# Performance work log

Hardware: AMD Instinct MI355X
Metric: run time of the kernel (lower is better)

## Reference

```python
import jax, jax.numpy as jnp
import numpy as np

IN_FEATURES = 4096
OUT_FEATURES = 16384
BATCH, SEQ = 4, 2048


def setup_inputs() -> dict:
    key = jax.random.key(0)
    k_x, k_w, k_b = jax.random.split(key, 3)
    x = jax.random.normal(k_x, (BATCH, SEQ, IN_FEATURES), dtype=jnp.float32)
    # int8-valued quantized weight stored as int32 for portability (values in [-128, 127])
    weight_quantized = jax.random.randint(k_w, (OUT_FEATURES, IN_FEATURES), -128, 128, dtype=jnp.int32)
    weight_scale = jnp.float32(0.01)        # scalar scale (symmetric quant)
    weight_zero_point = jnp.float32(0.0)    # scalar zero point
    bias = jax.random.normal(k_b, (OUT_FEATURES,), dtype=jnp.float32)
    return {
        "x": x,
        "weight_quantized": weight_quantized,
        "weight_scale": weight_scale,
        "weight_zero_point": weight_zero_point,
        "bias": bias,
    }


def reference(x, weight_quantized, weight_scale, weight_zero_point, bias):
    # dequantize: (q - zero_point) * scale  -> fp32 weight [out, in]
    weight = (weight_quantized.astype(jnp.float32) - weight_zero_point) * weight_scale
    # F.linear: y = x @ W^T + b ; x: [b, s, in], W: [out, in] -> y: [b, s, out]
    return jnp.einsum("bsi,oi->bso", x, weight) + bias
```

## Files before the change

kernel.cpp:

```cpp
#include <hip/hip_runtime.h>
#include <hip/hip_bf16.h>
#include <cstdint>


#define M_DIM 8192
#define N_DIM 16384
#define K_DIM 4096
#define BK    128
#define NT    (K_DIM / BK)

using i32x4 = __attribute__((ext_vector_type(4))) int;

__global__ __launch_bounds__(256) void quant_x_kernel(const float* __restrict__ x,
                                                      signed char* __restrict__ xq,
                                                      float* __restrict__ rs1,
                                                      float* __restrict__ rs2) {
    const int row = blockIdx.x;
    const float* xr = x + (size_t)row * K_DIM;
    const int tid = threadIdx.x;

    float4 v[4];
    float amax = 0.f;
    #pragma unroll
    for (int j = 0; j < 4; ++j) {
        v[j] = *(const float4*)(xr + j * 1024 + tid * 4);
        amax = fmaxf(amax, fmaxf(fmaxf(fabsf(v[j].x), fabsf(v[j].y)),
                                 fmaxf(fabsf(v[j].z), fabsf(v[j].w))));
    }
    #pragma unroll
    for (int off = 32; off > 0; off >>= 1)
        amax = fmaxf(amax, __shfl_xor(amax, off));
    __shared__ float smax[4];
    __shared__ int   ssum[4];
    const int wv = tid >> 6, ln = tid & 63;
    if (ln == 0) smax[wv] = amax;
    __syncthreads();
    amax = fmaxf(fmaxf(smax[0], smax[1]), fmaxf(smax[2], smax[3]));
    const float s   = amax * (1.0f / 127.0f);
    const float inv = amax > 0.f ? 127.0f / amax : 0.f;

    int sum = 0;
    #pragma unroll
    for (int j = 0; j < 4; ++j) {
        int q0 = (int)__builtin_rintf(v[j].x * inv);
        int q1 = (int)__builtin_rintf(v[j].y * inv);
        int q2 = (int)__builtin_rintf(v[j].z * inv);
        int q3 = (int)__builtin_rintf(v[j].w * inv);
        sum += q0 + q1 + q2 + q3;
        int packed = (q0 & 255) | ((q1 & 255) << 8) | ((q2 & 255) << 16) | ((q3 & 255) << 24);
        *(int*)(xq + (size_t)row * K_DIM + j * 1024 + tid * 4) = packed;
    }
    #pragma unroll
    for (int off = 32; off > 0; off >>= 1)
        sum += __shfl_xor(sum, off);
    if (ln == 0) ssum[wv] = sum;
    __syncthreads();
    if (tid == 0) {
        int t = ssum[0] + ssum[1] + ssum[2] + ssum[3];
        rs1[row] = s;
        rs2[row] = s * (float)t;
    }
}

__global__ void quant_w_kernel(const int* __restrict__ q, signed char* __restrict__ o,
                               long long n) {
    long long i = ((long long)blockIdx.x * blockDim.x + threadIdx.x) * 4;
    const long long stride = (long long)gridDim.x * blockDim.x * 4;
    for (; i < n; i += stride) {
        int4 v = *(const int4*)(q + i);
        int packed = (v.x & 255) | ((v.y & 255) << 8) | ((v.z & 255) << 16) | ((v.w & 255) << 24);
        *(int*)(o + i) = packed;
    }
}

#define SB() __builtin_amdgcn_sched_barrier(0)

__device__ __forceinline__ void barrier_() {
    SB();
    asm volatile("" ::: "memory");
    __builtin_amdgcn_s_barrier();
    asm volatile("" ::: "memory");
    SB();
}

__device__ __forceinline__ void stage_half(const signed char* g0, unsigned char* l0) {
    __builtin_amdgcn_global_load_lds((const __attribute__((address_space(1))) void*)g0,
                                     (__attribute__((address_space(3))) void*)l0, 16, 0, 0);
    __builtin_amdgcn_global_load_lds(
        (const __attribute__((address_space(1))) void*)(g0 + (size_t)64 * K_DIM),
        (__attribute__((address_space(3))) void*)(l0 + 8192), 16, 0, 0);
}

__global__ __launch_bounds__(512, 2) void gemm_i8_kernel(const signed char* __restrict__ A,
                                                         const signed char* __restrict__ B,
                                                         const float* __restrict__ rs1,
                                                         const float* __restrict__ rs2,
                                                         const float* __restrict__ scale,
                                                         const float* __restrict__ zpp,
                                                         const float* __restrict__ bias,
                                                         float* __restrict__ C) {
    extern __shared__ unsigned char smem[];

    const int tid  = threadIdx.x;
    const int wave = tid >> 6;
    const int lane = tid & 63;
    const int fr = lane & 15, kq = lane >> 4;
    const int wr = wave >> 2, wc = wave & 3;

    const int swz = (blockIdx.x & 7) * 256 + (blockIdx.x >> 3);
    const int ntn = N_DIM / 256;
    const int tileRow = (swz / ntn) * 256;
    const int tileCol = (swz % ntn) * 256;

    const size_t goff = (size_t)(tid >> 3) * K_DIM + (((tid & 7) ^ ((tid >> 3) & 7)) * 16);
    const signed char* Au  = A + (size_t)tileRow * K_DIM + goff;
    const signed char* Bu  = B + (size_t)tileCol * K_DIM + goff;
    const signed char* AuH = Au + (size_t)128 * K_DIM;
    const signed char* BuH = Bu + (size_t)128 * K_DIM;

    const int aoffB = wr * 16384 + fr * 128;
    const int boffB = 32768 + wc * 8192 + fr * 128;
    int cs[2];
    #pragma unroll
    for (int ks = 0; ks < 2; ++ks)
        cs[ks] = ((ks * 4 + kq) ^ (fr & 7)) * 16;

    i32x4 acc[8][4] = {};
    i32x4 arA[4][2], arB[4][2], b0r[2][2], b1r[2][2];

    {
        unsigned char* w0 = smem + wave * 1024;
        unsigned char* w1 = smem + 65536 + wave * 1024;
        stage_half(Au,  w0);
        stage_half(AuH, w0 + 16384);
        stage_half(Bu,  w0 + 32768);
        stage_half(BuH, w0 + 49152);
        stage_half(Bu + BK,  w1 + 32768);
        stage_half(BuH + BK, w1 + 49152);
        stage_half(Au + BK,  w1);
        stage_half(AuH + BK, w1 + 16384);
    }
    SB();
    asm volatile("s_waitcnt vmcnt(8)" ::: "memory");
    barrier_();
    #pragma unroll
    for (int m = 0; m < 4; ++m)
        #pragma unroll
        for (int ks = 0; ks < 2; ++ks)
            arA[m][ks] = *(const i32x4*)(smem + aoffB + m * 2048 + cs[ks]);
    #pragma unroll
    for (int n = 0; n < 2; ++n)
        #pragma unroll
        for (int ks = 0; ks < 2; ++ks)
            b0r[n][ks] = *(const i32x4*)(smem + boffB + n * 2048 + cs[ks]);
    SB();

    for (int t = 0; t < NT; ++t) {
        const unsigned char* sbr = smem + (t & 1) * 65536;
        const unsigned char* nxr = smem + ((t + 1) & 1) * 65536;
        unsigned char* sbw = smem + (t & 1) * 65536 + wave * 1024;
        const int kn2 = (t + 2) * BK;

        #pragma unroll
        for (int n = 0; n < 2; ++n)
            #pragma unroll
            for (int ks = 0; ks < 2; ++ks)
                b1r[n][ks] = *(const i32x4*)(sbr + boffB + (n + 2) * 2048 + cs[ks]);
        SB();
        asm volatile("s_waitcnt lgkmcnt(4)" ::: "memory");
        SB();
        __builtin_amdgcn_s_setprio(1);
        #pragma unroll
        for (int ks = 0; ks < 2; ++ks)
            #pragma unroll
            for (int m = 0; m < 4; ++m)
                #pragma unroll
                for (int n = 0; n < 2; ++n)
                    acc[m][n] = __builtin_amdgcn_mfma_i32_16x16x64_i8(arA[m][ks], b0r[n][ks], acc[m][n], 0, 0, 0);
        __builtin_amdgcn_s_setprio(0);
        barrier_();

        #pragma unroll
        for (int m = 0; m < 4; ++m)
            #pragma unroll
            for (int ks = 0; ks < 2; ++ks)
                arB[m][ks] = *(const i32x4*)(sbr + aoffB + (m + 4) * 2048 + cs[ks]);
        SB();
        asm volatile("s_waitcnt lgkmcnt(8)" ::: "memory");
        SB();
        __builtin_amdgcn_s_setprio(1);
        #pragma unroll
        for (int ks = 0; ks < 2; ++ks)
            #pragma unroll
            for (int m = 0; m < 4; ++m)
                #pragma unroll
                for (int n = 0; n < 2; ++n)
                    acc[m][n + 2] = __builtin_amdgcn_mfma_i32_16x16x64_i8(arA[m][ks], b1r[n][ks], acc[m][n + 2], 0, 0, 0);
        __builtin_amdgcn_s_setprio(0);
        barrier_();

        if (t + 2 < NT) {
            stage_half(Bu + kn2,  sbw + 32768);
            stage_half(BuH + kn2, sbw + 49152);
        }
        SB();
        asm volatile("s_waitcnt lgkmcnt(0)" ::: "memory");
        SB();
        __builtin_amdgcn_s_setprio(1);
        #pragma unroll
        for (int ks = 0; ks < 2; ++ks)
            #pragma unroll
            for (int m = 0; m < 4; ++m)
                #pragma unroll
                for (int n = 0; n < 2; ++n)
                    acc[m + 4][n + 2] = __builtin_amdgcn_mfma_i32_16x16x64_i8(arB[m][ks], b1r[n][ks], acc[m + 4][n + 2], 0, 0, 0);
        __builtin_amdgcn_s_setprio(0);
        SB();
        if (t + 2 < NT) {
            asm volatile("s_waitcnt vmcnt(4)" ::: "memory");
        } else {
            asm volatile("s_waitcnt vmcnt(0)" ::: "memory");
        }
        barrier_();

        if (t + 1 < NT) {
            #pragma unroll
            for (int m = 0; m < 4; ++m)
                #pragma unroll
                for (int ks = 0; ks < 2; ++ks)
                    arA[m][ks] = *(const i32x4*)(nxr + aoffB + m * 2048 + cs[ks]);
        }
        if (t + 2 < NT) {
            stage_half(Au + kn2,  sbw);
            stage_half(AuH + kn2, sbw + 16384);
        }
        SB();
        __builtin_amdgcn_s_setprio(1);
        #pragma unroll
        for (int ks = 0; ks < 2; ++ks)
            #pragma unroll
            for (int m = 0; m < 4; ++m)
                #pragma unroll
                for (int n = 0; n < 2; ++n)
                    acc[m + 4][n] = __builtin_amdgcn_mfma_i32_16x16x64_i8(arB[m][ks], b0r[n][ks], acc[m + 4][n], 0, 0, 0);
        __builtin_amdgcn_s_setprio(0);
        SB();
        if (t + 1 < NT) {
            #pragma unroll
            for (int n = 0; n < 2; ++n)
                #pragma unroll
                for (int ks = 0; ks < 2; ++ks)
                    b0r[n][ks] = *(const i32x4*)(nxr + boffB + n * 2048 + cs[ks]);
        }
        SB();
        barrier_();
    }

    const float sw  = scale[0];
    const float zpv = zpp[0];
    float bv[4];
    #pragma unroll
    for (int n = 0; n < 4; ++n)
        bv[n] = bias[tileCol + wc * 64 + n * 16 + fr];
    #pragma unroll
    for (int m = 0; m < 8; ++m) {
        #pragma unroll
        for (int j = 0; j < 4; ++j) {
            const int grow = tileRow + wr * 128 + m * 16 + kq * 4 + j;
            const float f1 = rs1[grow] * sw;
            const float f2 = zpv * rs2[grow] * sw;
            float* Crow = C + (size_t)grow * N_DIM + tileCol + wc * 64 + fr;
            #pragma unroll
            for (int n = 0; n < 4; ++n)
                Crow[n * 16] = f1 * (float)acc[m][n][j] - f2 + bv[n];
        }
    }
}

__global__ void gemm_naive(const float* __restrict__ x, const int* __restrict__ wq,
                           const float* __restrict__ sp, const float* __restrict__ zp,
                           const float* __restrict__ bias, float* __restrict__ out) {
    __shared__ float sX[32][33];
    __shared__ float sW[32][33];
    const float s = sp[0], z = zp[0];
    const int tx = threadIdx.x & 15, ty = threadIdx.x >> 4;
    const int row0 = blockIdx.y * 32, col0 = blockIdx.x * 32;
    float acc[2][2] = {};
    for (int k0 = 0; k0 < K_DIM; k0 += 32) {
        for (int i = threadIdx.x; i < 32 * 32; i += 256) {
            int r = i >> 5, cc2 = i & 31;
            sX[r][cc2] = x[(size_t)(row0 + r) * K_DIM + k0 + cc2];
            sW[r][cc2] = ((float)wq[(size_t)(col0 + r) * K_DIM + k0 + cc2] - z) * s;
        }
        __syncthreads();
        #pragma unroll
        for (int k = 0; k < 32; ++k) {
            float xa0 = sX[ty * 2][k], xa1 = sX[ty * 2 + 1][k];
            float wb0 = sW[tx * 2][k], wb1 = sW[tx * 2 + 1][k];
            acc[0][0] += xa0 * wb0; acc[0][1] += xa0 * wb1;
            acc[1][0] += xa1 * wb0; acc[1][1] += xa1 * wb1;
        }
        __syncthreads();
    }
    #pragma unroll
    for (int i = 0; i < 2; ++i)
        #pragma unroll
        for (int j = 0; j < 2; ++j)
            out[(size_t)(row0 + ty * 2 + i) * N_DIM + (col0 + tx * 2 + j)] =
                acc[i][j] + bias[col0 + tx * 2 + j];
}

extern "C" void kernel_launch(void* const* d_in, const int* in_sizes, int n_in,
                              void* d_out, int out_size, void* d_ws, size_t ws_size,
                              hipStream_t stream) {
    const float* x     = (const float*)d_in[0];
    const int*   wq    = (const int*)d_in[1];
    const float* scale = (const float*)d_in[2];
    const float* zp    = (const float*)d_in[3];
    const float* bias  = (const float*)d_in[4];
    float* out = (float*)d_out;

    const size_t offXq = 0;
    const size_t offWq = (size_t)M_DIM * K_DIM;
    const size_t offR1 = offWq + (size_t)N_DIM * K_DIM;
    const size_t offR2 = offR1 + (size_t)M_DIM * sizeof(float);
    const size_t need  = offR2 + (size_t)M_DIM * sizeof(float);

    if (ws_size >= need) {
        signed char* xq  = (signed char*)d_ws + offXq;
        signed char* wq8 = (signed char*)d_ws + offWq;
        float* rs1 = (float*)((char*)d_ws + offR1);
        float* rs2 = (float*)((char*)d_ws + offR2);
        quant_x_kernel<<<M_DIM, 256, 0, stream>>>(x, xq, rs1, rs2);
        quant_w_kernel<<<4096, 256, 0, stream>>>(wq, wq8, (long long)N_DIM * K_DIM);
        (void)hipFuncSetAttribute((const void*)gemm_i8_kernel,
                                  hipFuncAttributeMaxDynamicSharedMemorySize, 131072);
        gemm_i8_kernel<<<(M_DIM / 256) * (N_DIM / 256), 512, 131072, stream>>>(
            xq, wq8, rs1, rs2, scale, zp, bias, out);
    } else {
        dim3 grid(N_DIM / 32, M_DIM / 32);
        gemm_naive<<<grid, 256, 0, stream>>>(x, wq, scale, zp, bias, out);
    }
}
```

Baseline: 632.4 us.

## Restructure int8 GEMM main loop into per-k-half phases with smaller register fragments

The main loop now processes each BK tile as two k-halves. Each half loads only the A/B fragments it needs (arA[4], b0[2], etc.) instead of double-k fragments that were prefetched across iterations. This cuts register pressure. The cost is losing the cross-iteration LDS prefetch and adding more barriers and full lgkmcnt(0) waits per phase, which may leave the MFMA units exposed to LDS latency. The global stage prefetch and the vmcnt accounting are also adjusted.

```diff
diff --git a/kernel.cpp b/kernel.cpp
--- a/kernel.cpp
+++ b/kernel.cpp
@@ -122,11 +122,11 @@
     const int boffB = 32768 + wc * 8192 + fr * 128;
     int cs[2];
     #pragma unroll
-    for (int ks = 0; ks < 2; ++ks)
-        cs[ks] = ((ks * 4 + kq) ^ (fr & 7)) * 16;
+    for (int kh = 0; kh < 2; ++kh)
+        cs[kh] = ((kh * 4 + kq) ^ (fr & 7)) * 16;
 
     i32x4 acc[8][4] = {};
-    i32x4 arA[4][2], arB[4][2], b0r[2][2], b1r[2][2];
+    i32x4 arA[4], arB[4], b0[2], b1[2];
 
     {
         unsigned char* w0 = smem + wave * 1024;
@@ -143,120 +143,94 @@
     SB();
     asm volatile("s_waitcnt vmcnt(8)" ::: "memory");
     barrier_();
-    #pragma unroll
-    for (int m = 0; m < 4; ++m)
+
+    for (int t = 0; t < NT; ++t) {
+        const unsigned char* cb = smem + (t & 1) * 65536;
+        unsigned char* sw = smem + (t & 1) * 65536 + wave * 1024;
+        const int kn2 = (t + 2) * BK;
+        const bool st = (t + 2 < NT);
+
         #pragma unroll
-        for (int ks = 0; ks < 2; ++ks)
-            arA[m][ks] = *(const i32x4*)(smem + aoffB + m * 2048 + cs[ks]);
-    #pragma unroll
-    for (int n = 0; n < 2; ++n)
-        #pragma unroll
-        for (int ks = 0; ks < 2; ++ks)
-            b0r[n][ks] = *(const i32x4*)(smem + boffB + n * 2048 + cs[ks]);
-    SB();
-
-    for (int t = 0; t < NT; ++t) {
-        const unsigned char* sbr = smem + (t & 1) * 65536;
-        const unsigned char* nxr = smem + ((t + 1) & 1) * 65536;
-        unsigned char* sbw = smem + (t & 1) * 65536 + wave * 1024;
-        const int kn2 = (t + 2) * BK;
-
-        #pragma unroll
-        for (int n = 0; n < 2; ++n)
-            #pragma unroll
-            for (int ks = 0; ks < 2; ++ks)
-                b1r[n][ks] = *(const i32x4*)(sbr + boffB + (n + 2) * 2048 + cs[ks]);
-        SB();
-        asm volatile("s_waitcnt lgkmcnt(4)" ::: "memory");
-        SB();
-        __builtin_amdgcn_s_setprio(1);
-        #pragma unroll
-        for (int ks = 0; ks < 2; ++ks)
+        for (int kh = 0; kh < 2; ++kh) {
+            const int c = cs[kh];
+
+            #pragma unroll
+            for (int m = 0; m < 4; ++m)
+                arA[m] = *(const i32x4*)(cb + aoffB + m * 2048 + c);
+            #pragma unroll
+            for (int n = 0; n < 2; ++n)
+                b0[n] = *(const i32x4*)(cb + boffB + n * 2048 + c);
+            barrier_();
+            asm volatile("s_waitcnt lgkmcnt(0)" ::: "memory");
+            SB();
+            __builtin_amdgcn_s_setprio(1);
             #pragma unroll
             for (int m = 0; m < 4; ++m)
                 #pragma unroll
                 for (int n = 0; n < 2; ++n)
-                    acc[m][n] = __builtin_amdgcn_mfma_i32_16x16x64_i8(arA[m][ks], b0r[n][ks], acc[m][n], 0, 0, 0);
-        __builtin_amdgcn_s_setprio(0);
-        barrier_();
-
-        #pragma unroll
-        for (int m = 0; m < 4; ++m)
-            #pragma unroll
-            for (int ks = 0; ks < 2; ++ks)
-                arB[m][ks] = *(const i32x4*)(sbr + aoffB + (m + 4) * 2048 + cs[ks]);
-        SB();
-        asm volatile("s_waitcnt lgkmcnt(8)" ::: "memory");
-        SB();
-        __builtin_amdgcn_s_setprio(1);
-        #pragma unroll
-        for (int ks = 0; ks < 2; ++ks)
+                    acc[m][n] = __builtin_amdgcn_mfma_i32_16x16x64_i8(arA[m], b0[n], acc[m][n], 0, 0, 0);
+            __builtin_amdgcn_s_setprio(0);
+            barrier_();
+
+            #pragma unroll
+            for (int n = 0; n < 2; ++n)
+                b1[n] = *(const i32x4*)(cb + boffB + (n + 2) * 2048 + c);
+            barrier_();
+            asm volatile("s_waitcnt lgkmcnt(0)" ::: "memory");
+            SB();
+            __builtin_amdgcn_s_setprio(1);
             #pragma unroll
             for (int m = 0; m < 4; ++m)
                 #pragma unroll
                 for (int n = 0; n < 2; ++n)
-                    acc[m][n + 2] = __builtin_amdgcn_mfma_i32_16x16x64_i8(arA[m][ks], b1r[n][ks], acc[m][n + 2], 0, 0, 0);
-        __builtin_amdgcn_s_setprio(0);
-        barrier_();
-
-        if (t + 2 < NT) {
-            stage_half(Bu + kn2,  sbw + 32768);
-            stage_half(BuH + kn2, sbw + 49152);
-        }
-        SB();
-        asm volatile("s_waitcnt lgkmcnt(0)" ::: "memory");
-        SB();
-        __builtin_amdgcn_s_setprio(1);
-        #pragma unroll
-        for (int ks = 0; ks < 2; ++ks)
+                    acc[m][n + 2] = __builtin_amdgcn_mfma_i32_16x16x64_i8(arA[m], b1[n], acc[m][n + 2], 0, 0, 0);
+            __builtin_amdgcn_s_setprio(0);
+            barrier_();
+
+            #pragma unroll
+            for (int m = 0; m < 4; ++m)
+                arB[m] = *(const i32x4*)(cb + aoffB + (m + 4) * 2048 + c);
+            if (kh == 1 && st) {
+                stage_half(Bu + kn2,  sw + 32768);
+                stage_half(BuH + kn2, sw + 49152);
+            }
+            barrier_();
+            asm volatile("s_waitcnt lgkmcnt(0)" ::: "memory");
+            SB();
+            __builtin_amdgcn_s_setprio(1);
             #pragma unroll
             for (int m = 0; m < 4; ++m)
                 #pragma unroll
                 for (int n = 0; n < 2; ++n)
-                    acc[m + 4][n + 2] = __builtin_amdgcn_mfma_i32_16x16x64_i8(arB[m][ks], b1r[n][ks], acc[m + 4][n + 2], 0, 0, 0);
-        __builtin_amdgcn_s_setprio(0);
-        SB();
-        if (t + 2 < NT) {
-            asm volatile("s_waitcnt vmcnt(4)" ::: "memory");
-        } else {
-            asm volatile("s_waitcnt vmcnt(0)" ::: "memory");
-        }
-        barrier_();
-
-        if (t + 1 < NT) {
-            #pragma unroll
-            for (int m = 0; m < 4; ++m)
-                #pragma unroll
-                for (int ks = 0; ks < 2; ++ks)
-                    arA[m][ks] = *(const i32x4*)(nxr + aoffB + m * 2048 + cs[ks]);
-        }
-        if (t + 2 < NT) {
-            stage_half(Au + kn2,  sbw);
-            stage_half(AuH + kn2, sbw + 16384);
-        }
-        SB();
-        __builtin_amdgcn_s_setprio(1);
-        #pragma unroll
-        for (int ks = 0; ks < 2; ++ks)
+                    acc[m + 4][n + 2] = __builtin_amdgcn_mfma_i32_16x16x64_i8(arB[m], b1[n], acc[m + 4][n + 2], 0, 0, 0);
+            __builtin_amdgcn_s_setprio(0);
+            barrier_();
+
+            if (kh == 1 && st) {
+                stage_half(Au + kn2,  sw);
+                stage_half(AuH + kn2, sw + 16384);
+            }
+            barrier_();
+            __builtin_amdgcn_s_setprio(1);
             #pragma unroll
             for (int m = 0; m < 4; ++m)
                 #pragma unroll
                 for (int n = 0; n < 2; ++n)
-                    acc[m + 4][n] = __builtin_amdgcn_mfma_i32_16x16x64_i8(arB[m][ks], b0r[n][ks], acc[m + 4][n], 0, 0, 0);
-        __builtin_amdgcn_s_setprio(0);
-        SB();
-        if (t + 1 < NT) {
-            #pragma unroll
-            for (int n = 0; n < 2; ++n)
-                #pragma unroll
-                for (int ks = 0; ks < 2; ++ks)
-                    b0r[n][ks] = *(const i32x4*)(nxr + boffB + n * 2048 + cs[ks]);
+                    acc[m + 4][n] = __builtin_amdgcn_mfma_i32_16x16x64_i8(arB[m], b0[n], acc[m + 4][n], 0, 0, 0);
+            __builtin_amdgcn_s_setprio(0);
+            SB();
+            if (kh == 1) {
+                if (st) {
+                    asm volatile("s_waitcnt vmcnt(8)" ::: "memory");
+                } else if (t + 1 < NT) {
+                    asm volatile("s_waitcnt vmcnt(0)" ::: "memory");
+                }
+            }
+            barrier_();
         }
-        SB();
-        barrier_();
-    }
-
-    const float sw  = scale[0];
+    }
+
+    const float swv = scale[0];
     const float zpv = zpp[0];
     float bv[4];
     #pragma unroll
@@ -267,8 +241,8 @@
         #pragma unroll
         for (int j = 0; j < 4; ++j) {
             const int grow = tileRow + wr * 128 + m * 16 + kq * 4 + j;
-            const float f1 = rs1[grow] * sw;
-            const float f2 = zpv * rs2[grow] * sw;
+            const float f1 = rs1[grow] * swv;
+            const float f2 = zpv * rs2[grow] * swv;
             float* Crow = C + (size_t)grow * N_DIM + tileCol + wc * 64 + fr;
             #pragma unroll
             for (int n = 0; n < 4; ++n)
```

After: 681.8 us. +7.8%, slower.

## Merge quantization kernels and stage GEMM epilogue through LDS for vector stores

Applied to the files above, without the earlier changes.

The two preprocessing kernels (activation row quantization and weight int32-to-int8 packing) become one launch whose blocks branch on blockIdx, removing a kernel launch and letting both run concurrently. The GEMM epilogue now writes scaled accumulators to a per-wave LDS scratch region, then reads them back transposed so each lane issues 16-byte nontemporal stores of full row segments with a vectorized bias add. This replaces scattered 4-byte strided output stores with coalesced wide ones, at the cost of extra LDS traffic and waits, and it reuses the GEMM staging shared memory after the main loop.

```diff
diff --git a/kernel.cpp b/kernel.cpp
--- a/kernel.cpp
+++ b/kernel.cpp
@@ -10,66 +10,67 @@
 #define NT    (K_DIM / BK)
 
 using i32x4 = __attribute__((ext_vector_type(4))) int;
-
-__global__ __launch_bounds__(256) void quant_x_kernel(const float* __restrict__ x,
-                                                      signed char* __restrict__ xq,
-                                                      float* __restrict__ rs1,
-                                                      float* __restrict__ rs2) {
-    const int row = blockIdx.x;
-    const float* xr = x + (size_t)row * K_DIM;
+using f32x4 = __attribute__((ext_vector_type(4))) float;
+
+__global__ __launch_bounds__(256) void prep_kernel(const float* __restrict__ x,
+                                                   const int* __restrict__ q,
+                                                   signed char* __restrict__ xq,
+                                                   signed char* __restrict__ wq8,
+                                                   float* __restrict__ rs1,
+                                                   float* __restrict__ rs2) {
     const int tid = threadIdx.x;
-
-    float4 v[4];
-    float amax = 0.f;
-    #pragma unroll
-    for (int j = 0; j < 4; ++j) {
-        v[j] = *(const float4*)(xr + j * 1024 + tid * 4);
-        amax = fmaxf(amax, fmaxf(fmaxf(fabsf(v[j].x), fabsf(v[j].y)),
-                                 fmaxf(fabsf(v[j].z), fabsf(v[j].w))));
-    }
-    #pragma unroll
-    for (int off = 32; off > 0; off >>= 1)
-        amax = fmaxf(amax, __shfl_xor(amax, off));
-    __shared__ float smax[4];
-    __shared__ int   ssum[4];
-    const int wv = tid >> 6, ln = tid & 63;
-    if (ln == 0) smax[wv] = amax;
-    __syncthreads();
-    amax = fmaxf(fmaxf(smax[0], smax[1]), fmaxf(smax[2], smax[3]));
-    const float s   = amax * (1.0f / 127.0f);
-    const float inv = amax > 0.f ? 127.0f / amax : 0.f;
-
-    int sum = 0;
-    #pragma unroll
-    for (int j = 0; j < 4; ++j) {
-        int q0 = (int)__builtin_rintf(v[j].x * inv);
-        int q1 = (int)__builtin_rintf(v[j].y * inv);
-        int q2 = (int)__builtin_rintf(v[j].z * inv);
-        int q3 = (int)__builtin_rintf(v[j].w * inv);
-        sum += q0 + q1 + q2 + q3;
-        int packed = (q0 & 255) | ((q1 & 255) << 8) | ((q2 & 255) << 16) | ((q3 & 255) << 24);
-        *(int*)(xq + (size_t)row * K_DIM + j * 1024 + tid * 4) = packed;
-    }
-    #pragma unroll
-    for (int off = 32; off > 0; off >>= 1)
-        sum += __shfl_xor(sum, off);
-    if (ln == 0) ssum[wv] = sum;
-    __syncthreads();
-    if (tid == 0) {
-        int t = ssum[0] + ssum[1] + ssum[2] + ssum[3];
-        rs1[row] = s;
-        rs2[row] = s * (float)t;
-    }
-}
-
-__global__ void quant_w_kernel(const int* __restrict__ q, signed char* __restrict__ o,
-                               long long n) {
-    long long i = ((long long)blockIdx.x * blockDim.x + threadIdx.x) * 4;
-    const long long stride = (long long)gridDim.x * blockDim.x * 4;
-    for (; i < n; i += stride) {
-        int4 v = *(const int4*)(q + i);
-        int packed = (v.x & 255) | ((v.y & 255) << 8) | ((v.z & 255) << 16) | ((v.w & 255) << 24);
-        *(int*)(o + i) = packed;
+    if (blockIdx.x < M_DIM) {
+        const int row = blockIdx.x;
+        const float* xr = x + (size_t)row * K_DIM;
+        float4 v[4];
+        float amax = 0.f;
+        #pragma unroll
+        for (int j = 0; j < 4; ++j) {
+            v[j] = *(const float4*)(xr + j * 1024 + tid * 4);
+            amax = fmaxf(amax, fmaxf(fmaxf(fabsf(v[j].x), fabsf(v[j].y)),
+                                     fmaxf(fabsf(v[j].z), fabsf(v[j].w))));
+        }
+        #pragma unroll
+        for (int off = 32; off > 0; off >>= 1)
+            amax = fmaxf(amax, __shfl_xor(amax, off));
+        __shared__ float smax[4];
+        __shared__ int   ssum[4];
+        const int wv = tid >> 6, ln = tid & 63;
+        if (ln == 0) smax[wv] = amax;
+        __syncthreads();
+        amax = fmaxf(fmaxf(smax[0], smax[1]), fmaxf(smax[2], smax[3]));
+        const float s   = amax * (1.0f / 127.0f);
+        const float inv = amax > 0.f ? 127.0f / amax : 0.f;
+        int sum = 0;
+        #pragma unroll
+        for (int j = 0; j < 4; ++j) {
+            int q0 = (int)__builtin_rintf(v[j].x * inv);
+            int q1 = (int)__builtin_rintf(v[j].y * inv);
+            int q2 = (int)__builtin_rintf(v[j].z * inv);
+            int q3 = (int)__builtin_rintf(v[j].w * inv);
+            sum += q0 + q1 + q2 + q3;
+            int packed = (q0 & 255) | ((q1 & 255) << 8) | ((q2 & 255) << 16) | ((q3 & 255) << 24);
+            *(int*)(xq + (size_t)row * K_DIM + j * 1024 + tid * 4) = packed;
+        }
+        #pragma unroll
+        for (int off = 32; off > 0; off >>= 1)
+            sum += __shfl_xor(sum, off);
+        if (ln == 0) ssum[wv] = sum;
+        __syncthreads();
+        if (tid == 0) {
+            int t = ssum[0] + ssum[1] + ssum[2] + ssum[3];
+            rs1[row] = s;
+            rs2[row] = s * (float)t;
+        }
+    } else {
+        const long long n = (long long)N_DIM * K_DIM;
+        long long i = (((long long)(blockIdx.x - M_DIM)) * 256 + tid) * 4;
+        const long long stride = (long long)4096 * 256 * 4;
+        for (; i < n; i += stride) {
+            int4 v = *(const int4*)(q + i);
+            int packed = (v.x & 255) | ((v.y & 255) << 8) | ((v.z & 255) << 16) | ((v.w & 255) << 24);
+            *(int*)(wq8 + i) = packed;
+        }
     }
 }
 
@@ -256,24 +257,35 @@
         barrier_();
     }
 
-    const float sw  = scale[0];
+    float* tr = (float*)smem + wave * (16 * 68);
+    const float swv = scale[0];
     const float zpv = zpp[0];
-    float bv[4];
-    #pragma unroll
-    for (int n = 0; n < 4; ++n)
-        bv[n] = bias[tileCol + wc * 64 + n * 16 + fr];
     #pragma unroll
     for (int m = 0; m < 8; ++m) {
         #pragma unroll
         for (int j = 0; j < 4; ++j) {
-            const int grow = tileRow + wr * 128 + m * 16 + kq * 4 + j;
-            const float f1 = rs1[grow] * sw;
-            const float f2 = zpv * rs2[grow] * sw;
-            float* Crow = C + (size_t)grow * N_DIM + tileCol + wc * 64 + fr;
+            const int lrow = kq * 4 + j;
+            const int grow = tileRow + wr * 128 + m * 16 + lrow;
+            const float f1 = rs1[grow] * swv;
+            const float f2 = zpv * rs2[grow] * swv;
             #pragma unroll
             for (int n = 0; n < 4; ++n)
-                Crow[n * 16] = f1 * (float)acc[m][n][j] - f2 + bv[n];
-        }
+                tr[lrow * 68 + n * 16 + fr] = f1 * (float)acc[m][n][j] - f2;
+        }
+        asm volatile("s_waitcnt lgkmcnt(0)" ::: "memory");
+        SB();
+        #pragma unroll
+        for (int i = 0; i < 4; ++i) {
+            const int lrow = i * 4 + (lane >> 4);
+            f32x4 v = *(const f32x4*)(tr + lrow * 68 + (lane & 15) * 4);
+            const int grow = tileRow + wr * 128 + m * 16 + lrow;
+            const int gcol = tileCol + wc * 64 + (lane & 15) * 4;
+            f32x4 bv4 = *(const f32x4*)(bias + gcol);
+            v += bv4;
+            __builtin_nontemporal_store(v, (f32x4*)(C + (size_t)grow * N_DIM + gcol));
+        }
+        asm volatile("s_waitcnt lgkmcnt(0)" ::: "memory");
+        SB();
     }
 }
 
@@ -331,8 +343,7 @@
         signed char* wq8 = (signed char*)d_ws + offWq;
         float* rs1 = (float*)((char*)d_ws + offR1);
         float* rs2 = (float*)((char*)d_ws + offR2);
-        quant_x_kernel<<<M_DIM, 256, 0, stream>>>(x, xq, rs1, rs2);
-        quant_w_kernel<<<4096, 256, 0, stream>>>(wq, wq8, (long long)N_DIM * K_DIM);
+        prep_kernel<<<M_DIM + 4096, 256, 0, stream>>>(x, wq, xq, wq8, rs1, rs2);
         (void)hipFuncSetAttribute((const void*)gemm_i8_kernel,
                                   hipFuncAttributeMaxDynamicSharedMemorySize, 131072);
         gemm_i8_kernel<<<(M_DIM / 256) * (N_DIM / 256), 512, 131072, stream>>>(
```

After: 612.4 us. -3.2%, faster.
